# Kernel tuning notes

Measured on AMD Instinct MI355X. Metric: run time of the kernel, lower is better.

Reference implementation:

```python
import jax, jax.numpy as jnp
import numpy as np

H, DK, DV = 4, 64, 64        # heads, key/value head dims (hidden=256)
M, TOPK = 4, 2               # num memories, router top-k
GN, EPS, COND_SCALE = 16.0, 1e-5, 1.0


def setup_inputs() -> dict:
    key = jax.random.key(0)
    ks = jax.random.split(key, 12)
    B, Q, K, D = 8, 64, 256, 256
    w = lambda k, shape, fan: jax.random.normal(k, shape, jnp.float32) / np.sqrt(fan).astype(np.float32)
    return {
        "query": jax.random.normal(ks[0], (B, Q, D), jnp.float32),
        "keyval": jax.random.normal(ks[1], (B, K, D), jnp.float32),
        "attention_mask_kv": jnp.ones((B, K), jnp.int32),
        "W_cond": w(ks[2], (D, D), D),
        "W_q": w(ks[3], (D, H * DK), D),
        "W_k": w(ks[4], (D, H * DK), D),
        "W_v": w(ks[5], (D, H * DV), D),
        "W_gk1": w(ks[6], (D, 16), D),
        "W_gk2": w(ks[7], (16, H * DK), 16),
        "b_gk2": jnp.zeros((H * DK,), jnp.float32),
        "W_router": w(ks[8], (D, M), D),
        "norm_w": jnp.ones((DV,), jnp.float32),
        "W_o": w(ks[9], (H * DV, D), H * DV),
    }


def _mem_last(q_last, k, v, gk, sel, wgt):
    """Last-token output of one gated linear-attention memory.
    S_t = diag(exp(gk_t)) S_{t-1} + k_t v_t^T ; o_T = q_T S_T.
    q_last: (N,H,DK); k,gk: (N,K,H,DK); v: (N,K,H,DV); sel,wgt: (N,K)."""
    k_e = k * sel[:, :, None, None]
    v_e = v * wgt[:, :, None, None]
    gk_e = gk * sel[:, :, None, None]          # unselected tokens: no decay, no update
    G = jnp.cumsum(gk_e, axis=1)               # (N,K,H,DK), log decays
    decay = jnp.exp(G[:, -1:, :, :] - G)       # remaining decay to last step, <= 1
    s = jnp.einsum('nhd,nthd->nth', q_last, k_e * decay)
    return jnp.einsum('nth,nthv->nhv', s, v_e)


def reference(query, keyval, attention_mask_kv, W_cond, W_q, W_k, W_v,
              W_gk1, W_gk2, b_gk2, W_router, norm_w, W_o):
    B, Q, D = query.shape
    K = keyval.shape[1]
    N = B * Q
    # broadcast KV expansion + cond injection
    cond = (query @ W_cond) * COND_SCALE                         # (B,Q,D)
    x = (keyval[:, None, :, :] + cond[:, :, None, :]).reshape(N, K, D)
    m = jnp.broadcast_to(attention_mask_kv[:, None, :].astype(x.dtype), (B, Q, K)).reshape(N, K)
    # projections
    q = (x @ W_q).reshape(N, K, H, DK)
    k = (x @ W_k).reshape(N, K, H, DK) * m[:, :, None, None]
    v = (x @ W_v).reshape(N, K, H, DV) * m[:, :, None, None]
    gk = (jax.nn.log_sigmoid(x @ W_gk1 @ W_gk2 + b_gk2) / GN).reshape(N, K, H, DK)
    gk = gk * m[:, :, None, None]
    # router: softmax -> top-k -> renormalize
    router_logits = (x @ W_router).reshape(N * K, M)
    probs = jax.nn.softmax(router_logits, axis=-1)
    topv, topi = jax.lax.top_k(probs, TOPK)
    topv = topv / jnp.sum(topv, axis=-1, keepdims=True)
    w_mem = jnp.sum(jax.nn.one_hot(topi, M, dtype=x.dtype) * topv[..., None], axis=-2)
    w_mem = w_mem.reshape(N, K, M)
    # shared memory (always on) + routed memories
    q_last = q[:, -1]
    ones = jnp.ones((N, K), x.dtype)
    o = _mem_last(q_last, k, v, gk, ones, ones)
    for e in range(M):
        we = w_mem[:, :, e]
        o = o + _mem_last(q_last, k, v, gk, (we > 0).astype(x.dtype), we)
    # per-head RMSNorm + output projection
    o = o * jax.lax.rsqrt(jnp.mean(o * o, axis=-1, keepdims=True) + EPS) * norm_w
    out = (o.reshape(N, H * DV) @ W_o).reshape(B, Q, D)
    return out, router_logits
```

## Files before the change

### kernel.cpp

```cpp
#include <hip/hip_runtime.h>
#include <math.h>

#define Hh   4
#define Bb   8
#define Qq   64
#define Kk   256
#define Dd   256
#define Nn   (Bb * Qq)
#define GNf  16.0f
#define EPSf 1e-5f

#define SKV  832
#define SCB  1088

struct GemmS { float As[16][136]; float Ws[16][136]; };
struct RtrS  { float WrT[4][260]; };
union  WorkS { GemmS g; RtrS r; };

__device__ __forceinline__ float wred(float x) {
#pragma unroll
    for (int off = 32; off > 0; off >>= 1)
        x += __shfl_xor(x, off, 64);
    return x;
}

__global__ __launch_bounds__(256) void prep(
    const float* __restrict__ Wg1, const float* __restrict__ Wg2,
    float* __restrict__ Wg)
{
    const int e = blockIdx.x * 256 + threadIdx.x;
    const int k = e >> 8, c = e & 255;
    float s = 0.f;
#pragma unroll
    for (int i = 0; i < 16; ++i)
        s = fmaf(Wg1[k * 16 + i], Wg2[i * 256 + c], s);
    Wg[e] = s;
}

__device__ void gemm64(GemmS& g, const float* __restrict__ A, int lda, int Mv,
                       const float* __restrict__ B, int bn,
                       float* __restrict__ C, int ldc)
{
    float (*As)[68] = (float(*)[68])(&g.As[0][0]);
    const int tid = threadIdx.x;
    const int ty = tid >> 4, tx = tid & 15;
    const int am = tid >> 2, ak = (tid & 3) << 2;
    const int wk = tid >> 4, wc = (tid & 15) << 3;
    const int ams = (am < Mv) ? am : (Mv - 1);

    float acc[4][8] = {};
    const float* aptr = A + (size_t)ams * lda + ak;
    const float* bptr = B + wk * 256 + bn + wc;
    float4 av = *(const float4*)aptr;
    float4 b0 = *(const float4*)bptr;
    float4 b1 = *(const float4*)(bptr + 4);

    for (int k0 = 0; k0 < 256; k0 += 16) {
        __syncthreads();
        As[ak + 0][am] = av.x; As[ak + 1][am] = av.y;
        As[ak + 2][am] = av.z; As[ak + 3][am] = av.w;
        *(float4*)&g.Ws[wk][wc]     = b0;
        *(float4*)&g.Ws[wk][wc + 4] = b1;
        __syncthreads();
        if (k0 + 16 < 256) {
            av = *(const float4*)(aptr + k0 + 16);
            b0 = *(const float4*)(bptr + (k0 + 16) * 256);
            b1 = *(const float4*)(bptr + (k0 + 16) * 256 + 4);
        }
#pragma unroll
        for (int kk = 0; kk < 16; ++kk) {
            const float4 a4 = *(const float4*)&As[kk][ty << 2];
            const float4 w0 = *(const float4*)&g.Ws[kk][tx << 2];
            const float4 w1 = *(const float4*)&g.Ws[kk][64 + (tx << 2)];
            const float a_[4] = {a4.x, a4.y, a4.z, a4.w};
            const float w_[8] = {w0.x, w0.y, w0.z, w0.w, w1.x, w1.y, w1.z, w1.w};
#pragma unroll
            for (int i = 0; i < 4; ++i)
#pragma unroll
                for (int jj = 0; jj < 8; ++jj)
                    acc[i][jj] = fmaf(a_[i], w_[jj], acc[i][jj]);
        }
    }

#pragma unroll
    for (int i = 0; i < 4; ++i) {
        const int rr = (ty << 2) + i;
        if (rr < Mv) {
            *(float4*)(C + (size_t)rr * ldc + (tx << 2)) =
                make_float4(acc[i][0], acc[i][1], acc[i][2], acc[i][3]);
            *(float4*)(C + (size_t)rr * ldc + 64 + (tx << 2)) =
                make_float4(acc[i][4], acc[i][5], acc[i][6], acc[i][7]);
        }
    }
}

__device__ void router_region(RtrS& rs, const float* __restrict__ A,
                              const float* __restrict__ Wr,
                              float* __restrict__ C, int ldc, int row0)
{
    const int tid = threadIdx.x;
    for (int idx = tid; idx < 1024; idx += 256)
        rs.WrT[idx & 3][idx >> 2] = Wr[idx];
    __syncthreads();
    const int row = row0 + (tid >> 2), c = tid & 3;
    const float* a = A + (size_t)row * 256;
    float acc = 0.f;
#pragma unroll 8
    for (int k4 = 0; k4 < 64; ++k4) {
        const float4 avv = *(const float4*)(a + (k4 << 2));
        const float4 wvv = *(const float4*)&rs.WrT[c][k4 << 2];
        acc = fmaf(avv.x, wvv.x, acc);
        acc = fmaf(avv.y, wvv.y, acc);
        acc = fmaf(avv.z, wvv.z, acc);
        acc = fmaf(avv.w, wvv.w, acc);
    }
    C[(size_t)row * ldc + c] = acc;
}

__global__ __launch_bounds__(256) void gemm_main(
    const float* __restrict__ keyval, const float* __restrict__ query,
    const float* __restrict__ W_k, const float* __restrict__ W_v,
    const float* __restrict__ Wg, const float* __restrict__ W_cond,
    const float* __restrict__ W_q, const float* __restrict__ W_router,
    float* __restrict__ KVb, float* __restrict__ cond,
    float* __restrict__ qlast)
{
    __shared__ WorkS S;
    const int id = blockIdx.x;
    if (id < 210) {
        const float* A; int lda, Mv; const float* Bm; int bn; float* C; int ldc;
        if (id < 192) {
            const int rt = id / 6, ct = id % 6;
            const float* Bsel; int cbase;
            if (ct < 2)      { Bsel = W_k; cbase = 0; }
            else if (ct < 4) { Bsel = W_v; cbase = 256; }
            else             { Bsel = Wg;  cbase = 512; }
            A = keyval + (size_t)rt * 64 * 256; lda = 256; Mv = 64;
            Bm = Bsel; bn = (ct & 1) * 128;
            C = KVb + (size_t)rt * 64 * SKV + cbase + bn; ldc = SKV;
        } else if (id < 208) {
            const int t = id - 192, rt = t >> 1, ct = t & 1;
            A = query + (size_t)rt * 64 * 256; lda = 256; Mv = 64;
            Bm = W_cond; bn = ct * 128;
            C = cond + (size_t)rt * 64 * 256 + ct * 128; ldc = 256;
        } else {
            const int ct = id - 208;
            A = keyval + 255 * 256; lda = Kk * Dd; Mv = 8;
            Bm = W_q; bn = ct * 128;
            C = qlast + ct * 128; ldc = 256;
        }
        gemm64(S.g, A, lda, Mv, Bm, bn, C, ldc);
    } else {
        router_region(S.r, keyval, W_router, KVb + 768, SKV, (id - 210) * 64);
    }
}

__global__ __launch_bounds__(256) void gemm_cb(
    const float* __restrict__ cond,
    const float* __restrict__ W_q, const float* __restrict__ W_k,
    const float* __restrict__ W_v, const float* __restrict__ Wg,
    const float* __restrict__ W_router, float* __restrict__ Cb)
{
    __shared__ WorkS S;
    const int id = blockIdx.x;
    if (id < 64) {
        const int rg = id >> 4, t = id & 15, rt = t >> 1, ct = t & 1;
        const float* Bsel = (rg == 0) ? W_q : (rg == 1) ? W_k
                          : (rg == 2) ? W_v : Wg;
        gemm64(S.g, cond + (size_t)rt * 64 * 256, 256, 64,
               Bsel, ct * 128,
               Cb + (size_t)rt * 64 * SCB + rg * 256 + ct * 128, SCB);
    } else {
        router_region(S.r, cond, W_router, Cb + 1024, SCB, (id - 64) * 64);
    }
}

__global__ __launch_bounds__(256) void mom_fused(
    const float* __restrict__ KVb, const float* __restrict__ Cb,
    const float* __restrict__ qlast, const float* __restrict__ b_gk2,
    const int* __restrict__ mask, const float* __restrict__ W_o,
    const float* __restrict__ norm_w, float* __restrict__ out,
    float* __restrict__ logits)
{
    __shared__ float4 wm[Kk];
    __shared__ float  Pt[4][16][68];
    __shared__ float  sbuf[4][16];
    __shared__ float  onorm[Dd];

    const int n = blockIdx.x;
    const int b = n >> 6;
    const int j = threadIdx.x;
    const int lane = j & 63;
    const int wv = j >> 6;

    const float qc = Cb[(size_t)n * SCB + j];
    const float kc = Cb[(size_t)n * SCB + 256 + j];
    const float vc = Cb[(size_t)n * SCB + 512 + j];
    const float pc = Cb[(size_t)n * SCB + 768 + j] + b_gk2[j];
    const float4 rc = *(const float4*)(Cb + (size_t)n * SCB + 1024);

    const int* pm = mask + b * Kk;

    {
        const float4 kvr = *(const float4*)(KVb + (size_t)(b * Kk + j) * SKV + 768);
        float l[4] = {kvr.x + rc.x, kvr.y + rc.y, kvr.z + rc.z, kvr.w + rc.w};
        *(float4*)(logits + ((size_t)n * Kk + j) * 4) =
            make_float4(l[0], l[1], l[2], l[3]);

        int i1 = 0;
#pragma unroll
        for (int q = 1; q < 4; ++q) if (l[q] > l[i1]) i1 = q;
        int i2 = -1;
#pragma unroll
        for (int q = 0; q < 4; ++q) {
            if (q == i1) continue;
            if (i2 < 0 || l[q] > l[i2]) i2 = q;
        }
        const float mx = fmaxf(l[i1], l[i2]);
        const float e1 = __expf(l[i1] - mx);
        const float e2 = __expf(l[i2] - mx);
        const float inv = 1.f / (e1 + e2);
        float w[4] = {0.f, 0.f, 0.f, 0.f};
        w[i1] = e1 * inv;
        w[i2] = e2 * inv;
        wm[j] = make_float4(w[0], w[1], w[2], w[3]);
    }
    __syncthreads();

    const float ql  = qlast[b * 256 + j] + qc;
    const float qkc = ql * kc;
    const float* pk = KVb + (size_t)b * Kk * SKV + j;
    const float* pv = pk + 256;
    const float* pp = pk + 512;

    float E0 = 1.f, E1 = 1.f, E2 = 1.f, E3 = 1.f, E4 = 1.f;
    float o = 0.f;
    const int tl = lane & 15, qg = lane >> 4;

    for (int t0 = Kk - 16; t0 >= 0; t0 -= 16) {
        float vreg[16];
#pragma unroll
        for (int i = 0; i < 16; ++i) {
            const int t = t0 + 15 - i;
            const float mf   = (float)pm[t];
            const float kraw = pk[(size_t)t * SKV];
            const float vraw = pv[(size_t)t * SKV];
            const float praw = pp[(size_t)t * SKV];
            const float pre  = praw + pc;

            const float ls = fminf(pre, 0.f)
                           - __logf(1.f + __expf(-fabsf(pre)));
            const float dg = __expf(ls * (0.0625f * mf));

            const float4 w  = wm[t];
            const float zf = E0 + w.x * E1 + w.y * E2 + w.z * E3 + w.w * E4;
            Pt[wv][i][lane] = fmaf(ql, kraw, qkc) * zf * mf;
            vreg[i] = vraw + vc;

            E0 *= dg;
            E1 *= (w.x > 0.f) ? dg : 1.f;
            E2 *= (w.y > 0.f) ? dg : 1.f;
            E3 *= (w.z > 0.f) ? dg : 1.f;
            E4 *= (w.w > 0.f) ? dg : 1.f;
        }
        __builtin_amdgcn_wave_barrier();

        float s = 0.f;
#pragma unroll
        for (int rr4 = 0; rr4 < 4; ++rr4) {
            const float4 p4 = *(const float4*)&Pt[wv][tl][qg * 16 + rr4 * 4];
            s += (p4.x + p4.y) + (p4.z + p4.w);
        }
        s += __shfl_xor(s, 16, 64);
        s += __shfl_xor(s, 32, 64);
        sbuf[wv][tl] = s;
        __builtin_amdgcn_wave_barrier();
#pragma unroll
        for (int rr4 = 0; rr4 < 4; ++rr4) {
            const float4 sv = *(const float4*)&sbuf[wv][rr4 * 4];
            o = fmaf(sv.x, vreg[rr4 * 4 + 0], o);
            o = fmaf(sv.y, vreg[rr4 * 4 + 1], o);
            o = fmaf(sv.z, vreg[rr4 * 4 + 2], o);
            o = fmaf(sv.w, vreg[rr4 * 4 + 3], o);
        }
    }

    const float ms = wred(o * o) * (1.0f / 64.0f);
    onorm[j] = o * rsqrtf(ms + EPSf) * norm_w[lane];
    __syncthreads();

    float acc = 0.f;
#pragma unroll 8
    for (int k = 0; k < 256; ++k)
        acc = fmaf(onorm[k], W_o[(size_t)k * 256 + j], acc);
    out[(size_t)n * 256 + j] = acc;
}

extern "C" void kernel_launch(void* const* d_in, const int* in_sizes, int n_in,
                              void* d_out, int out_size, void* d_ws, size_t ws_size,
                              hipStream_t stream)
{
    const float* query    = (const float*)d_in[0];
    const float* keyval   = (const float*)d_in[1];
    const int*   mask     = (const int*)  d_in[2];
    const float* W_cond   = (const float*)d_in[3];
    const float* W_q      = (const float*)d_in[4];
    const float* W_k      = (const float*)d_in[5];
    const float* W_v      = (const float*)d_in[6];
    const float* W_gk1    = (const float*)d_in[7];
    const float* W_gk2    = (const float*)d_in[8];
    const float* b_gk2    = (const float*)d_in[9];
    const float* W_router = (const float*)d_in[10];
    const float* norm_w   = (const float*)d_in[11];
    const float* W_o      = (const float*)d_in[12];

    float* out    = (float*)d_out;
    float* logits = out + Nn * Dd;

    float* p = (float*)d_ws;
    float* Wg    = p; p += 256 * 256;
    float* KVb   = p; p += 2048 * SKV;
    float* cond  = p; p += Nn * 256;
    float* qlast = p; p += 8 * 256;
    float* Cb    = p; p += Nn * SCB;

    prep<<<256, dim3(256), 0, stream>>>(W_gk1, W_gk2, Wg);

    gemm_main<<<242, dim3(256), 0, stream>>>(
        keyval, query, W_k, W_v, Wg, W_cond, W_q, W_router, KVb, cond, qlast);

    gemm_cb<<<72, dim3(256), 0, stream>>>(cond, W_q, W_k, W_v, Wg, W_router, Cb);

    mom_fused<<<Nn, dim3(256), 0, stream>>>(
        KVb, Cb, qlast, b_gk2, mask, W_o, norm_w, out, logits);
}
```

Measured before the change: 221.3 us.

## Precompose W_cond into projection weights and merge GEMM stages

```diff
diff --git a/kernel.cpp b/kernel.cpp
--- a/kernel.cpp
+++ b/kernel.cpp
@@ -15,26 +15,15 @@
 
 struct GemmS { float As[16][136]; float Ws[16][136]; };
 struct RtrS  { float WrT[4][260]; };
+struct WcbgS { float Wg1s[256][16]; float Ts[256][16]; };
 union  WorkS { GemmS g; RtrS r; };
+union  P0S   { GemmS g; RtrS r; WcbgS w; };
 
 __device__ __forceinline__ float wred(float x) {
 #pragma unroll
     for (int off = 32; off > 0; off >>= 1)
         x += __shfl_xor(x, off, 64);
     return x;
-}
-
-__global__ __launch_bounds__(256) void prep(
-    const float* __restrict__ Wg1, const float* __restrict__ Wg2,
-    float* __restrict__ Wg)
-{
-    const int e = blockIdx.x * 256 + threadIdx.x;
-    const int k = e >> 8, c = e & 255;
-    float s = 0.f;
-#pragma unroll
-    for (int i = 0; i < 16; ++i)
-        s = fmaf(Wg1[k * 16 + i], Wg2[i * 256 + c], s);
-    Wg[e] = s;
 }
 
 __device__ void gemm64(GemmS& g, const float* __restrict__ A, int lda, int Mv,
@@ -117,61 +106,157 @@
     C[(size_t)row * ldc + c] = acc;
 }
 
-__global__ __launch_bounds__(256) void gemm_main(
+__device__ void wg_region(const float* __restrict__ Wg1,
+                          const float* __restrict__ Wg2,
+                          float* __restrict__ Wg, int k0)
+{
+    const int c = threadIdx.x;
+    float w2[16];
+#pragma unroll
+    for (int i = 0; i < 16; ++i) w2[i] = Wg2[i * 256 + c];
+#pragma unroll
+    for (int r = 0; r < 16; ++r) {
+        const int k = k0 + r;
+        float s = 0.f;
+#pragma unroll
+        for (int i = 0; i < 16; ++i) s = fmaf(Wg1[k * 16 + i], w2[i], s);
+        Wg[k * 256 + c] = s;
+    }
+}
+
+__device__ void wcbg_region(WcbgS& w, const float* __restrict__ W_cond,
+                            const float* __restrict__ Wg1,
+                            const float* __restrict__ Wg2,
+                            float* __restrict__ Wcbg, int colbase)
+{
+    const int tid = threadIdx.x;
+    for (int idx = tid; idx < 4096; idx += 256)
+        ((float*)w.Wg1s)[idx] = Wg1[idx];
+    __syncthreads();
+
+    {
+        float acc[16] = {};
+        const float* arow = W_cond + (size_t)tid * 256;
+        for (int k4 = 0; k4 < 64; ++k4) {
+            const float4 a = *(const float4*)(arow + (k4 << 2));
+            const float av[4] = {a.x, a.y, a.z, a.w};
+#pragma unroll
+            for (int kk = 0; kk < 4; ++kk) {
+                const int k = (k4 << 2) + kk;
+                const float4 g0 = *(const float4*)&w.Wg1s[k][0];
+                const float4 g1 = *(const float4*)&w.Wg1s[k][4];
+                const float4 g2 = *(const float4*)&w.Wg1s[k][8];
+                const float4 g3 = *(const float4*)&w.Wg1s[k][12];
+                acc[0]  = fmaf(av[kk], g0.x, acc[0]);
+                acc[1]  = fmaf(av[kk], g0.y, acc[1]);
+                acc[2]  = fmaf(av[kk], g0.z, acc[2]);
+                acc[3]  = fmaf(av[kk], g0.w, acc[3]);
+                acc[4]  = fmaf(av[kk], g1.x, acc[4]);
+                acc[5]  = fmaf(av[kk], g1.y, acc[5]);
+                acc[6]  = fmaf(av[kk], g1.z, acc[6]);
+                acc[7]  = fmaf(av[kk], g1.w, acc[7]);
+                acc[8]  = fmaf(av[kk], g2.x, acc[8]);
+                acc[9]  = fmaf(av[kk], g2.y, acc[9]);
+                acc[10] = fmaf(av[kk], g2.z, acc[10]);
+                acc[11] = fmaf(av[kk], g2.w, acc[11]);
+                acc[12] = fmaf(av[kk], g3.x, acc[12]);
+                acc[13] = fmaf(av[kk], g3.y, acc[13]);
+                acc[14] = fmaf(av[kk], g3.z, acc[14]);
+                acc[15] = fmaf(av[kk], g3.w, acc[15]);
+            }
+        }
+#pragma unroll
+        for (int e4 = 0; e4 < 4; ++e4)
+            *(float4*)&w.Ts[tid][e4 << 2] =
+                make_float4(acc[e4 * 4], acc[e4 * 4 + 1],
+                            acc[e4 * 4 + 2], acc[e4 * 4 + 3]);
+    }
+    __syncthreads();
+
+    const int c = colbase + (tid & 127);
+    const int r0 = (tid >> 7) * 128;
+    float wg2c[16];
+#pragma unroll
+    for (int e = 0; e < 16; ++e) wg2c[e] = Wg2[e * 256 + c];
+    for (int r = r0; r < r0 + 128; ++r) {
+        const float4 t0 = *(const float4*)&w.Ts[r][0];
+        const float4 t1 = *(const float4*)&w.Ts[r][4];
+        const float4 t2 = *(const float4*)&w.Ts[r][8];
+        const float4 t3 = *(const float4*)&w.Ts[r][12];
+        float s = 0.f;
+        s = fmaf(t0.x, wg2c[0],  s); s = fmaf(t0.y, wg2c[1],  s);
+        s = fmaf(t0.z, wg2c[2],  s); s = fmaf(t0.w, wg2c[3],  s);
+        s = fmaf(t1.x, wg2c[4],  s); s = fmaf(t1.y, wg2c[5],  s);
+        s = fmaf(t1.z, wg2c[6],  s); s = fmaf(t1.w, wg2c[7],  s);
+        s = fmaf(t2.x, wg2c[8],  s); s = fmaf(t2.y, wg2c[9],  s);
+        s = fmaf(t2.z, wg2c[10], s); s = fmaf(t2.w, wg2c[11], s);
+        s = fmaf(t3.x, wg2c[12], s); s = fmaf(t3.y, wg2c[13], s);
+        s = fmaf(t3.z, wg2c[14], s); s = fmaf(t3.w, wg2c[15], s);
+        Wcbg[(size_t)r * 256 + c] = s;
+    }
+}
+
+__global__ __launch_bounds__(256) void k_p0(
+    const float* __restrict__ W_cond, const float* __restrict__ W_q,
+    const float* __restrict__ W_k, const float* __restrict__ W_v,
+    const float* __restrict__ W_gk1, const float* __restrict__ W_gk2,
+    const float* __restrict__ W_router,
+    float* __restrict__ Wcb_q, float* __restrict__ Wcb_k,
+    float* __restrict__ Wcb_v, float* __restrict__ Wcb_g,
+    float* __restrict__ Wcb_r, float* __restrict__ Wg)
+{
+    __shared__ P0S S;
+    const int id = blockIdx.x;
+    if (id < 24) {
+        const int rg = id >> 3, t = id & 7, rt = t >> 1, ct = t & 1;
+        const float* Bsel = (rg == 0) ? W_q : (rg == 1) ? W_k : W_v;
+        float* Csel = (rg == 0) ? Wcb_q : (rg == 1) ? Wcb_k : Wcb_v;
+        gemm64(S.g, W_cond + (size_t)rt * 64 * 256, 256, 64,
+               Bsel, ct * 128,
+               Csel + (size_t)rt * 64 * 256 + ct * 128, 256);
+    } else if (id < 26) {
+        wcbg_region(S.w, W_cond, W_gk1, W_gk2, Wcb_g, (id - 24) * 128);
+    } else if (id < 30) {
+        router_region(S.r, W_cond, W_router, Wcb_r, 4, (id - 26) * 64);
+    } else {
+        wg_region(W_gk1, W_gk2, Wg, (id - 30) * 16);
+    }
+}
+
+__global__ __launch_bounds__(256) void k_p1(
     const float* __restrict__ keyval, const float* __restrict__ query,
     const float* __restrict__ W_k, const float* __restrict__ W_v,
-    const float* __restrict__ Wg, const float* __restrict__ W_cond,
-    const float* __restrict__ W_q, const float* __restrict__ W_router,
-    float* __restrict__ KVb, float* __restrict__ cond,
+    const float* __restrict__ Wg, const float* __restrict__ W_q,
+    const float* __restrict__ W_router,
+    const float* __restrict__ Wcb_q, const float* __restrict__ Wcb_k,
+    const float* __restrict__ Wcb_v, const float* __restrict__ Wcb_g,
+    const float* __restrict__ Wcb_r,
+    float* __restrict__ KVb, float* __restrict__ Cb,
     float* __restrict__ qlast)
 {
     __shared__ WorkS S;
     const int id = blockIdx.x;
-    if (id < 210) {
-        const float* A; int lda, Mv; const float* Bm; int bn; float* C; int ldc;
-        if (id < 192) {
-            const int rt = id / 6, ct = id % 6;
-            const float* Bsel; int cbase;
-            if (ct < 2)      { Bsel = W_k; cbase = 0; }
-            else if (ct < 4) { Bsel = W_v; cbase = 256; }
-            else             { Bsel = Wg;  cbase = 512; }
-            A = keyval + (size_t)rt * 64 * 256; lda = 256; Mv = 64;
-            Bm = Bsel; bn = (ct & 1) * 128;
-            C = KVb + (size_t)rt * 64 * SKV + cbase + bn; ldc = SKV;
-        } else if (id < 208) {
-            const int t = id - 192, rt = t >> 1, ct = t & 1;
-            A = query + (size_t)rt * 64 * 256; lda = 256; Mv = 64;
-            Bm = W_cond; bn = ct * 128;
-            C = cond + (size_t)rt * 64 * 256 + ct * 128; ldc = 256;
-        } else {
-            const int ct = id - 208;
-            A = keyval + 255 * 256; lda = Kk * Dd; Mv = 8;
-            Bm = W_q; bn = ct * 128;
-            C = qlast + ct * 128; ldc = 256;
-        }
-        gemm64(S.g, A, lda, Mv, Bm, bn, C, ldc);
-    } else {
-        router_region(S.r, keyval, W_router, KVb + 768, SKV, (id - 210) * 64);
-    }
-}
-
-__global__ __launch_bounds__(256) void gemm_cb(
-    const float* __restrict__ cond,
-    const float* __restrict__ W_q, const float* __restrict__ W_k,
-    const float* __restrict__ W_v, const float* __restrict__ Wg,
-    const float* __restrict__ W_router, float* __restrict__ Cb)
-{
-    __shared__ WorkS S;
-    const int id = blockIdx.x;
-    if (id < 64) {
-        const int rg = id >> 4, t = id & 15, rt = t >> 1, ct = t & 1;
-        const float* Bsel = (rg == 0) ? W_q : (rg == 1) ? W_k
-                          : (rg == 2) ? W_v : Wg;
-        gemm64(S.g, cond + (size_t)rt * 64 * 256, 256, 64,
+    if (id < 192) {
+        const int rt = id / 6, ct = id % 6;
+        const float* Bsel = (ct < 2) ? W_k : (ct < 4) ? W_v : Wg;
+        gemm64(S.g, keyval + (size_t)rt * 64 * 256, 256, 64,
+               Bsel, (ct & 1) * 128,
+               KVb + (size_t)rt * 64 * SKV + (ct >> 1) * 256 + (ct & 1) * 128,
+               SKV);
+    } else if (id < 224) {
+        router_region(S.r, keyval, W_router, KVb + 768, SKV, (id - 192) * 64);
+    } else if (id < 288) {
+        const int t = id - 224, rg = t >> 4, tt = t & 15, rt = tt >> 1, ct = tt & 1;
+        const float* Bsel = (rg == 0) ? Wcb_q : (rg == 1) ? Wcb_k
+                          : (rg == 2) ? Wcb_v : Wcb_g;
+        gemm64(S.g, query + (size_t)rt * 64 * 256, 256, 64,
                Bsel, ct * 128,
                Cb + (size_t)rt * 64 * SCB + rg * 256 + ct * 128, SCB);
+    } else if (id < 296) {
+        router_region(S.r, query, Wcb_r, Cb + 1024, SCB, (id - 288) * 64);
     } else {
-        router_region(S.r, cond, W_router, Cb + 1024, SCB, (id - 64) * 64);
+        gemm64(S.g, keyval + 255 * 256, Kk * Dd, 8, W_q, (id - 296) * 128,
+               qlast + (id - 296) * 128, 256);
     }
 }
 
@@ -248,9 +333,10 @@
             const float praw = pp[(size_t)t * SKV];
             const float pre  = praw + pc;
 
-            const float ls = fminf(pre, 0.f)
-                           - __logf(1.f + __expf(-fabsf(pre)));
-            const float dg = __expf(ls * (0.0625f * mf));
+            const float y   = pre * 1.44269504f;
+            const float t1  = __builtin_amdgcn_exp2f(-fabsf(y));
+            const float ls2 = fminf(y, 0.f) - __builtin_amdgcn_logf(1.f + t1);
+            const float dg  = __builtin_amdgcn_exp2f(ls2 * (0.0625f * mf));
 
             const float4 w  = wm[t];
             const float zf = E0 + w.x * E1 + w.y * E2 + w.z * E3 + w.w * E4;
@@ -319,17 +405,22 @@
 
     float* p = (float*)d_ws;
     float* Wg    = p; p += 256 * 256;
+    float* Wcb_q = p; p += 256 * 256;
+    float* Wcb_k = p; p += 256 * 256;
+    float* Wcb_v = p; p += 256 * 256;
+    float* Wcb_g = p; p += 256 * 256;
+    float* Wcb_r = p; p += 256 * 4;
     float* KVb   = p; p += 2048 * SKV;
-    float* cond  = p; p += Nn * 256;
     float* qlast = p; p += 8 * 256;
     float* Cb    = p; p += Nn * SCB;
 
-    prep<<<256, dim3(256), 0, stream>>>(W_gk1, W_gk2, Wg);
-
-    gemm_main<<<242, dim3(256), 0, stream>>>(
-        keyval, query, W_k, W_v, Wg, W_cond, W_q, W_router, KVb, cond, qlast);
-
-    gemm_cb<<<72, dim3(256), 0, stream>>>(cond, W_q, W_k, W_v, Wg, W_router, Cb);
+    k_p0<<<46, dim3(256), 0, stream>>>(
+        W_cond, W_q, W_k, W_v, W_gk1, W_gk2, W_router,
+        Wcb_q, Wcb_k, Wcb_v, Wcb_g, Wcb_r, Wg);
+
+    k_p1<<<298, dim3(256), 0, stream>>>(
+        keyval, query, W_k, W_v, Wg, W_q, W_router,
+        Wcb_q, Wcb_k, Wcb_v, Wcb_g, Wcb_r, KVb, Cb, qlast);
 
     mom_fused<<<Nn, dim3(256), 0, stream>>>(
         KVb, Cb, qlast, b_gk2, mask, W_o, norm_w, out, logits);
```

After: 250.0 us. 13.0% more time.
